# Optimization experiments

Measured on AMD Instinct MI355X. Metric: run time of the kernel, lower is better.

The kernel has to match this reference:

```python
import jax, jax.numpy as jnp
import numpy as np

S = 4096
D_MODEL = 1024
D_INTERNAL = 4096


def setup_inputs() -> dict:
    key = jax.random.key(0)
    ks = jax.random.split(key, 12)
    s = 0.02
    return {
        "x": jax.random.normal(ks[0], (S, D_MODEL), dtype=jnp.float32),
        # projection weights stored as [d_in, d_out] so y = x @ W + b
        "Wq": jax.random.normal(ks[1], (D_MODEL, D_MODEL), dtype=jnp.float32) * s,
        "bq": jnp.zeros((D_MODEL,), dtype=jnp.float32),
        "Wk": jax.random.normal(ks[2], (D_MODEL, D_MODEL), dtype=jnp.float32) * s,
        "bk": jnp.zeros((D_MODEL,), dtype=jnp.float32),
        "Wv": jax.random.normal(ks[3], (D_MODEL, D_MODEL), dtype=jnp.float32) * s,
        "bv": jnp.zeros((D_MODEL,), dtype=jnp.float32),
        "W1": jax.random.normal(ks[4], (D_MODEL, D_INTERNAL), dtype=jnp.float32) * s,
        "b1": jnp.zeros((D_INTERNAL,), dtype=jnp.float32),
        "W2": jax.random.normal(ks[5], (D_INTERNAL, D_MODEL), dtype=jnp.float32) * s,
        "b2": jnp.zeros((D_MODEL,), dtype=jnp.float32),
    }


def reference(x, Wq, bq, Wk, bk, Wv, bv, W1, b1, W2, b2):
    # x: [S, D] (module is unbatched: k.transpose(0,1) implies 2-D input)
    d_model = x.shape[-1]
    q = x @ Wq + bq                         # [S, D]
    k = x @ Wk + bk                         # [S, D]
    v = x @ Wv + bv                         # [S, D]
    scores = (q @ k.T) / jnp.sqrt(jnp.asarray(d_model, x.dtype))  # [S, S]
    s = x.shape[0]
    causal = jnp.triu(jnp.ones((s, s), dtype=bool), k=1)           # True above diag
    scores = jnp.where(causal, jnp.asarray(-1e9, x.dtype), scores)
    attn = jax.nn.softmax(scores, axis=-1)  # [S, S]
    attended = attn @ v                     # [S, D]
    h = x + attended                        # residual 1
    ff = jax.nn.relu(h @ W1 + b1) @ W2 + b2 # 2-layer MLP
    out = h + ff                            # residual 2
    return (out, attn)
```

## Files before the change

### kernel.cpp

```cpp
#include <hip/hip_runtime.h>
#include <hip/hip_bf16.h>


typedef __attribute__((ext_vector_type(4))) float  f32x4;
typedef __attribute__((ext_vector_type(8))) short  bf16x8;
typedef __attribute__((ext_vector_type(4))) unsigned short us4;
typedef __attribute__((ext_vector_type(8))) unsigned short us8;

#define DEVINL __device__ __forceinline__

static constexpr int S   = 4096;
static constexpr int DM  = 1024;
static constexpr int DI  = 4096;

DEVINL unsigned short f2bf(float f) {
  union { float f; unsigned u; } v; v.f = f;
  unsigned r = v.u + 0x7fffu + ((v.u >> 16) & 1u);
  return (unsigned short)(r >> 16);
}

DEVINL float bf2f(unsigned short b) {
  union { unsigned u; float f; } v; v.u = ((unsigned)b) << 16;
  return v.f;
}

DEVINL void gld_lds16(const unsigned short* g, unsigned short* l) {
  __builtin_amdgcn_global_load_lds(
      (const __attribute__((address_space(1))) void*)g,
      (__attribute__((address_space(3))) void*)l,
      16, 0, 0);
}

DEVINL int xcd_remap(int orig, int nwg) {
  const int q = nwg >> 3, r = nwg & 7;
  const int x = orig & 7, idx = orig >> 3;
  return (x < r ? x * (q + 1) : r * (q + 1) + (x - r) * q) + idx;
}

__global__ void prep_all(const float* __restrict__ x,
                         const float* __restrict__ Wq,
                         const float* __restrict__ Wk,
                         const float* __restrict__ Wv,
                         const float* __restrict__ W1,
                         const float* __restrict__ W2,
                         const float* __restrict__ bq,
                         const float* __restrict__ bk,
                         const float* __restrict__ bv,
                         unsigned short* __restrict__ xb,
                         unsigned short* __restrict__ Wqkvt,
                         unsigned short* __restrict__ W1t,
                         unsigned short* __restrict__ W2t,
                         float* __restrict__ bqkv) {
  __shared__ float tile[32][33];
  const int b = blockIdx.x;
  const int tid = threadIdx.x;

  if (b < 2048) {
    long i = ((long)b * 256 + tid) * 8;
    f32x4 a = *(const f32x4*)(x + i);
    f32x4 c = *(const f32x4*)(x + i + 4);
    us8 o;
    o[0] = f2bf(a[0]); o[1] = f2bf(a[1]); o[2] = f2bf(a[2]); o[3] = f2bf(a[3]);
    o[4] = f2bf(c[0]); o[5] = f2bf(c[1]); o[6] = f2bf(c[2]); o[7] = f2bf(c[3]);
    *(us8*)(xb + i) = o;
    return;
  }
  if (b >= 13312) {
    const int t = b - 13312;
    const float* src = (t == 0) ? bq : (t == 1) ? bk : bv;
    const int i = tid * 4;
    *(f32x4*)(bqkv + t * DM + i) = *(const f32x4*)(src + i);
    return;
  }

  const float* in; unsigned short* out; int R, C, t;
  if (b < 3072)      { in = Wq; out = Wqkvt;                      R = DM; C = DM; t = b - 2048; }
  else if (b < 4096) { in = Wk; out = Wqkvt + (size_t)DM * DM;    R = DM; C = DM; t = b - 3072; }
  else if (b < 5120) { in = Wv; out = Wqkvt + 2 * (size_t)DM * DM;R = DM; C = DM; t = b - 4096; }
  else if (b < 9216) { in = W1; out = W1t;                        R = DM; C = DI; t = b - 5120; }
  else               { in = W2; out = W2t;                        R = DI; C = DM; t = b - 9216; }
  const int gx = C >> 5;
  const int bx = (t % gx) * 32, by = (t / gx) * 32;
  const int tx = tid & 31, ty = tid >> 5;
  #pragma unroll
  for (int j = 0; j < 4; ++j) {
    int r = ty + j * 8;
    tile[r][tx] = in[(size_t)(by + r) * C + bx + tx];
  }
  __syncthreads();
  #pragma unroll
  for (int j = 0; j < 4; ++j) {
    int r = ty + j * 8;
    out[(size_t)(bx + r) * R + by + tx] = f2bf(tile[tx][r]);
  }
}

__global__ void transpose_bf16(const unsigned short* __restrict__ in, int ld,
                               unsigned short* __restrict__ out, int ldo) {
  __shared__ unsigned short tile[32][33];
  const int bx = blockIdx.x * 32, by = blockIdx.y * 32;
  const int tx = threadIdx.x, ty = threadIdx.y;
  #pragma unroll
  for (int j = 0; j < 4; ++j) {
    int r = ty + j * 8;
    tile[r][tx] = in[(size_t)(by + r) * ld + bx + tx];
  }
  __syncthreads();
  #pragma unroll
  for (int j = 0; j < 4; ++j) {
    int r = ty + j * 8;
    out[(size_t)(bx + r) * ldo + by + tx] = tile[tx][r];
  }
}

enum { EPI_QKV = 0, EPI_SCE = 1, EPI_FF1 = 4, EPI_PART = 6 };

#define VM_WAIT0 asm volatile("s_waitcnt vmcnt(0)" ::: "memory")

template <int EPI, bool TRI_PACK, bool TRI_TRUNC>
__launch_bounds__(256, 2)
__global__ void gemm4(const unsigned short* __restrict__ A,
                      const unsigned short* __restrict__ Bt,
                      int M, int N, int K, int lda, int ldb, int kChunk, int GX,
                      const float* __restrict__ bias,
                      float* __restrict__ Cf,
                      unsigned short* __restrict__ Cb,
                      float scale) {
  const int wg = xcd_remap(blockIdx.x, gridDim.x);
  int bm, bn;
  if (TRI_PACK) {
    int t = wg;
    bm = (int)((sqrtf(8.f * (float)t + 1.f) - 1.f) * 0.5f);
    while ((bm + 1) * (bm + 2) / 2 <= t) ++bm;
    while (bm * (bm + 1) / 2 > t) --bm;
    bn = t - bm * (bm + 1) / 2;
  } else {
    const int GY_ = gridDim.x / GX;
    const int bpp = GY_ * 8;
    const int panel = wg / bpp, rem = wg % bpp;
    bm = rem >> 3;
    bn = panel * 8 + (rem & 7);
  }
  const int bm0 = bm * 128, bn0 = bn * 128;

  const int kbeg = blockIdx.z * kChunk;
  int kend = min(K, kbeg + kChunk);
  if (TRI_TRUNC) kend = min(kend, bm0 + 128);
  const int len = kend - kbeg;
  const int NT = (len > 0) ? (len >> 6) : 0;

  __shared__ __align__(16) unsigned short lds[2 * 16384];

  const int tid  = threadIdx.x;
  const int lane = tid & 63;
  const int w    = tid >> 6;
  const int wr   = w >> 1, wc = w & 1;
  const int fr   = lane & 15, fq = lane >> 4;

  f32x4 acc[4][4] = {};

  const int tq = tid >> 2;
  const int swcolE = ((tid & 3) * 8) ^ ((tq & 6) << 2);
  const unsigned short* gA = A  + (size_t)(bm0 + tq) * lda + kbeg + swcolE;
  const unsigned short* gB = Bt + (size_t)(bn0 + tq) * ldb + kbeg + swcolE;
  const size_t aH = (size_t)64 * lda, bH = (size_t)64 * ldb;

  auto stage = [&](int buf, int t_) {
    unsigned short* base = (unsigned short*)lds + buf * 16384;
    const size_t go = (size_t)t_ * 64;
    #pragma unroll
    for (int ks = 0; ks < 2; ++ks) {
      const size_t gk = go + ks * 32;
      gld_lds16(gA + gk,      base + ks * 4096 + w * 512);
      gld_lds16(gA + aH + gk, base + ks * 4096 + 2048 + w * 512);
      gld_lds16(gB + gk,      base + 8192 + ks * 4096 + w * 512);
      gld_lds16(gB + bH + gk, base + 8192 + ks * 4096 + 2048 + w * 512);
    }
  };

  const int frSw = (fq * 8) ^ ((fr & 6) << 2);
  auto rdA = [&](int buf, int ks, int mi) {
    return *(const bf16x8*)((const unsigned short*)lds + buf * 16384 + ks * 4096 +
                            (wr * 64 + mi * 16 + fr) * 32 + frSw);
  };
  auto rdB = [&](int buf, int ks, int ni) {
    return *(const bf16x8*)((const unsigned short*)lds + buf * 16384 + 8192 + ks * 4096 +
                            (wc * 64 + ni * 16 + fr) * 32 + frSw);
  };

  if (NT > 0) {
    stage(0, 0);
    VM_WAIT0;
    __builtin_amdgcn_s_barrier();

    for (int t = 0; t < NT; ++t) {
      const int cur = t & 1, nxt = cur ^ 1;
      const bool pf = (t + 1 < NT);
      if (pf) stage(nxt, t + 1);

      #pragma unroll
      for (int ks = 0; ks < 2; ++ks) {
        bf16x8 a[4], b[4];
        #pragma unroll
        for (int mi = 0; mi < 4; ++mi) a[mi] = rdA(cur, ks, mi);
        #pragma unroll
        for (int ni = 0; ni < 4; ++ni) b[ni] = rdB(cur, ks, ni);
        #pragma unroll
        for (int mi = 0; mi < 4; ++mi)
          #pragma unroll
          for (int ni = 0; ni < 4; ++ni)
            acc[mi][ni] = __builtin_amdgcn_mfma_f32_16x16x32_bf16(
                a[mi], b[ni], acc[mi][ni], 0, 0, 0);
      }

      if (pf) { VM_WAIT0; }
      __builtin_amdgcn_s_barrier();
    }
  }

  const int row0 = bm0 + wr * 64 + fq * 4;
  const int col0 = bn0 + wc * 64 + fr;
  const size_t zoff = (EPI == EPI_PART) ? (size_t)blockIdx.z * M * N : 0;
  #pragma unroll
  for (int ni = 0; ni < 4; ++ni) {
    const int col = col0 + ni * 16;
    float bval = 0.f;
    if (EPI == EPI_QKV || EPI == EPI_FF1) bval = bias[col];
    #pragma unroll
    for (int mi = 0; mi < 4; ++mi) {
      #pragma unroll
      for (int j = 0; j < 4; ++j) {
        const int row = row0 + mi * 16 + j;
        const size_t idx = zoff + (size_t)row * N + col;
        const float c = acc[mi][ni][j];
        if (EPI == EPI_QKV) {
          Cb[idx] = f2bf(c + bval);
        } else if (EPI == EPI_SCE) {
          const float e = (col <= row) ? __expf(c * scale) : 0.f;
          Cb[idx] = f2bf(e);
        } else if (EPI == EPI_FF1) {
          const float r = c + bval;
          Cb[idx] = f2bf(r > 0.f ? r : 0.f);
        } else {
          Cf[idx] = c;
        }
      }
    }
  }
}

__global__ void normalize_rows(const unsigned short* __restrict__ attnb,
                               float* __restrict__ attnf,
                               float* __restrict__ rowsum) {
  const int m = blockIdx.x;
  const int tid = threadIdx.x;
  const int valid = m + 1;
  const unsigned short* rowb = attnb + (size_t)m * S;
  float* rowf = attnf + (size_t)m * S;

  float v[4][4];
  float lsum = 0.f;
  #pragma unroll
  for (int i = 0; i < 4; ++i) {
    const int idx = tid * 4 + i * 1024;
    #pragma unroll
    for (int j = 0; j < 4; ++j) v[i][j] = 0.f;
    if (i * 1024 <= m) {
      us4 b = *(const us4*)(rowb + idx);
      #pragma unroll
      for (int j = 0; j < 4; ++j) {
        const float e = (idx + j < valid) ? bf2f(b[j]) : 0.f;
        v[i][j] = e;
        lsum += e;
      }
    }
  }
  #pragma unroll
  for (int off = 32; off > 0; off >>= 1)
    lsum += __shfl_xor(lsum, off, 64);

  __shared__ float red[4];
  if ((tid & 63) == 0) red[tid >> 6] = lsum;
  __syncthreads();
  const float total = red[0] + red[1] + red[2] + red[3];
  if (tid == 0) rowsum[m] = total;
  const float inv = 1.0f / total;

  #pragma unroll
  for (int i = 0; i < 4; ++i) {
    const int idx = tid * 4 + i * 1024;
    f32x4 o;
    #pragma unroll
    for (int j = 0; j < 4; ++j) o[j] = v[i][j] * inv;
    *(f32x4*)(rowf + idx) = o;
  }
}

template <bool FINAL, bool NORM>
__global__ void reduce_k(const float* __restrict__ P,
                         const float* __restrict__ res,
                         const float* __restrict__ bias,
                         const float* __restrict__ rowsum,
                         float* __restrict__ outf,
                         unsigned short* __restrict__ outb, long n) {
  long i = ((long)blockIdx.x * 256 + threadIdx.x) * 4;
  if (i >= n) return;
  f32x4 a = *(const f32x4*)(P + i);
  f32x4 b = *(const f32x4*)(P + n + i);
  f32x4 r = *(const f32x4*)(res + i);
  float inv = 1.f;
  if (NORM) inv = 1.0f / rowsum[i >> 10];
  if (FINAL) {
    f32x4 bb = *(const f32x4*)(bias + (i & (DM - 1)));
    f32x4 o;
    #pragma unroll
    for (int j = 0; j < 4; ++j) o[j] = a[j] + b[j] + r[j] + bb[j];
    *(f32x4*)(outf + i) = o;
  } else {
    f32x4 o; us4 ob;
    #pragma unroll
    for (int j = 0; j < 4; ++j) {
      o[j] = (a[j] + b[j]) * inv + r[j];
      ob[j] = f2bf(o[j]);
    }
    *(f32x4*)(outf + i) = o;
    *(us4*)(outb + i) = ob;
  }
}

extern "C" void kernel_launch(void* const* d_in, const int* in_sizes, int n_in,
                              void* d_out, int out_size, void* d_ws, size_t ws_size,
                              hipStream_t stream) {
  const float* x  = (const float*)d_in[0];
  const float* Wq = (const float*)d_in[1];
  const float* bq = (const float*)d_in[2];
  const float* Wk = (const float*)d_in[3];
  const float* bk = (const float*)d_in[4];
  const float* Wv = (const float*)d_in[5];
  const float* bv = (const float*)d_in[6];
  const float* W1 = (const float*)d_in[7];
  const float* b1 = (const float*)d_in[8];
  const float* W2 = (const float*)d_in[9];
  const float* b2 = (const float*)d_in[10];
  (void)in_sizes; (void)n_in; (void)out_size; (void)ws_size;

  float* outp  = (float*)d_out;
  float* attnf = (float*)d_out + (size_t)S * DM;

  const size_t MB = 1ull << 20;
  char* ws = (char*)d_ws;
  unsigned short* W2t   = (unsigned short*)(ws + 0 * MB);
  unsigned short* W1t   = (unsigned short*)(ws + 8 * MB);
  float*          h     = (float*)(ws + 16 * MB);
  unsigned short* hb    = (unsigned short*)(ws + 32 * MB);
  unsigned short* vt    = (unsigned short*)(ws + 40 * MB);
  unsigned short* attnb = (unsigned short*)(ws + 48 * MB);
  unsigned short* qkv   = (unsigned short*)(ws + 80 * MB);
  unsigned short* xb    = (unsigned short*)(ws + 104 * MB);
  unsigned short* Wqkvt = (unsigned short*)(ws + 112 * MB);
  float*          bqkv  = (float*)(ws + 118 * MB);
  float*          rowsum= (float*)(ws + 119 * MB);
  unsigned short* ff1b  = (unsigned short*)(ws + 40 * MB);
  float*          Ppv   = (float*)(ws + 80 * MB);
  float*          Pff   = (float*)(ws + 72 * MB);

  prep_all<<<dim3(13315), 256, 0, stream>>>(
      x, Wq, Wk, Wv, W1, W2, bq, bk, bv, xb, Wqkvt, W1t, W2t, bqkv);

  gemm4<EPI_QKV, false, false><<<dim3((S / 128) * (3072 / 128), 1, 1), 256, 0, stream>>>(
      xb, Wqkvt, S, 3072, DM, DM, DM, DM, 3072 / 128, bqkv, nullptr, qkv, 1.f);
  transpose_bf16<<<dim3(DM / 32, S / 32), dim3(32, 8), 0, stream>>>(
      qkv + 2 * DM, 3072, vt, S);

  gemm4<EPI_SCE, true, false><<<dim3(528, 1, 1), 256, 0, stream>>>(
      qkv, qkv + DM, S, S, DM, 3072, 3072, DM, 0, nullptr, nullptr, attnb, 0.03125f);

  normalize_rows<<<dim3(S), 256, 0, stream>>>(attnb, attnf, rowsum);

  gemm4<EPI_PART, false, true><<<dim3((S / 128) * (DM / 128), 1, 2), 256, 0, stream>>>(
      attnb, vt, S, DM, S, S, S, S / 2, DM / 128, nullptr, Ppv, nullptr, 1.f);
  reduce_k<false, true><<<dim3((S * DM) / 1024), 256, 0, stream>>>(
      Ppv, x, nullptr, rowsum, h, hb, (long)S * DM);

  gemm4<EPI_FF1, false, false><<<dim3((S / 128) * (DI / 128), 1, 1), 256, 0, stream>>>(
      hb, W1t, S, DI, DM, DM, DM, DM, DI / 128, b1, nullptr, ff1b, 1.f);

  gemm4<EPI_PART, false, false><<<dim3((S / 128) * (DM / 128), 1, 2), 256, 0, stream>>>(
      ff1b, W2t, S, DM, DI, DI, DI, DI / 2, DM / 128, nullptr, Pff, nullptr, 1.f);
  reduce_k<true, false><<<dim3((S * DM) / 1024), 256, 0, stream>>>(
      Pff, h, b2, nullptr, outp, nullptr, (long)S * DM);
}
```

Baseline: 240.9 us.

## Replace 128x128 GEMM with 256x256 8-wave ping-pong pipelined kernel

Grows the GEMM tile from 128x128 with 4 waves to 256x256 with 8 waves. The main loop is split into four sub-phases that interleave LDS reads, staged global-to-LDS loads two tiles ahead, barriers, and MFMA bursts raised with s_setprio. Partial vmcnt waits replace the full drains. The aim is more data reuse per tile and overlap of memory traffic with matrix math. The cost is fewer workgroups (e.g. 136 triangle tiles for scores), more registers and LDS per block, and more barriers per iteration.

```diff
diff --git a/kernel.cpp b/kernel.cpp
--- a/kernel.cpp
+++ b/kernel.cpp
@@ -115,17 +115,20 @@
 
 enum { EPI_QKV = 0, EPI_SCE = 1, EPI_FF1 = 4, EPI_PART = 6 };
 
+#define VM_WAIT6 asm volatile("s_waitcnt vmcnt(6)" ::: "memory")
 #define VM_WAIT0 asm volatile("s_waitcnt vmcnt(0)" ::: "memory")
+#define LGKM0    do { asm volatile("s_waitcnt lgkmcnt(0)" ::: "memory"); \
+                      __builtin_amdgcn_sched_barrier(0); } while (0)
 
 template <int EPI, bool TRI_PACK, bool TRI_TRUNC>
-__launch_bounds__(256, 2)
-__global__ void gemm4(const unsigned short* __restrict__ A,
-                      const unsigned short* __restrict__ Bt,
-                      int M, int N, int K, int lda, int ldb, int kChunk, int GX,
-                      const float* __restrict__ bias,
-                      float* __restrict__ Cf,
-                      unsigned short* __restrict__ Cb,
-                      float scale) {
+__launch_bounds__(512, 2)
+__global__ void gemm8p(const unsigned short* __restrict__ A,
+                       const unsigned short* __restrict__ Bt,
+                       int M, int N, int K, int lda, int ldb, int kChunk, int GX,
+                       const float* __restrict__ bias,
+                       float* __restrict__ Cf,
+                       unsigned short* __restrict__ Cb,
+                       float scale) {
   const int wg = xcd_remap(blockIdx.x, gridDim.x);
   int bm, bn;
   if (TRI_PACK) {
@@ -134,91 +137,125 @@
     while ((bm + 1) * (bm + 2) / 2 <= t) ++bm;
     while (bm * (bm + 1) / 2 > t) --bm;
     bn = t - bm * (bm + 1) / 2;
-  } else {
-    const int GY_ = gridDim.x / GX;
-    const int bpp = GY_ * 8;
-    const int panel = wg / bpp, rem = wg % bpp;
-    bm = rem >> 3;
-    bn = panel * 8 + (rem & 7);
-  }
-  const int bm0 = bm * 128, bn0 = bn * 128;
+  } else { bm = wg / GX; bn = wg % GX; }
+  const int bm0 = bm * 256, bn0 = bn * 256;
 
   const int kbeg = blockIdx.z * kChunk;
   int kend = min(K, kbeg + kChunk);
-  if (TRI_TRUNC) kend = min(kend, bm0 + 128);
-  const int len = kend - kbeg;
-  const int NT = (len > 0) ? (len >> 6) : 0;
-
-  __shared__ __align__(16) unsigned short lds[2 * 16384];
+  if (TRI_TRUNC) kend = min(kend, bm0 + 256);
+  const int NT = (kend > kbeg) ? ((kend - kbeg) >> 6) : 0;
+
+  __shared__ __align__(16) unsigned short lds[2 * 32768];
 
   const int tid  = threadIdx.x;
   const int lane = tid & 63;
   const int w    = tid >> 6;
-  const int wr   = w >> 1, wc = w & 1;
+  const int wr   = w >> 2, wc = w & 3;
   const int fr   = lane & 15, fq = lane >> 4;
 
-  f32x4 acc[4][4] = {};
-
-  const int tq = tid >> 2;
-  const int swcolE = ((tid & 3) * 8) ^ ((tq & 6) << 2);
-  const unsigned short* gA = A  + (size_t)(bm0 + tq) * lda + kbeg + swcolE;
-  const unsigned short* gB = Bt + (size_t)(bn0 + tq) * ldb + kbeg + swcolE;
-  const size_t aH = (size_t)64 * lda, bH = (size_t)64 * ldb;
-
-  auto stage = [&](int buf, int t_) {
-    unsigned short* base = (unsigned short*)lds + buf * 16384;
-    const size_t go = (size_t)t_ * 64;
-    #pragma unroll
-    for (int ks = 0; ks < 2; ++ks) {
-      const size_t gk = go + ks * 32;
-      gld_lds16(gA + gk,      base + ks * 4096 + w * 512);
-      gld_lds16(gA + aH + gk, base + ks * 4096 + 2048 + w * 512);
-      gld_lds16(gB + gk,      base + 8192 + ks * 4096 + w * 512);
-      gld_lds16(gB + bH + gk, base + 8192 + ks * 4096 + 2048 + w * 512);
-    }
+  f32x4 acc[8][4] = {};
+
+  const int srow   = tid >> 2;
+  const int swcolE = ((tid & 3) * 8) ^ ((srow & 6) << 2);
+  const unsigned short* gA = A  + (size_t)(bm0 + srow) * lda + kbeg + swcolE;
+  const unsigned short* gB = Bt + (size_t)(bn0 + srow) * ldb + kbeg + swcolE;
+  const size_t aH = (size_t)128 * lda, bH = (size_t)128 * ldb;
+
+  auto stA = [&](int buf, int t_, int ks) {
+    unsigned short* dst = (unsigned short*)lds + buf * 32768 + ks * 16384 + w * 512;
+    const size_t go = (size_t)t_ * 64 + ks * 32;
+    gld_lds16(gA + go,      dst);
+    gld_lds16(gA + aH + go, dst + 4096);
+  };
+  auto stB = [&](int buf, int t_, int ks) {
+    unsigned short* dst = (unsigned short*)lds + buf * 32768 + 8192 + ks * 16384 + w * 512;
+    const size_t go = (size_t)t_ * 64 + ks * 32;
+    gld_lds16(gB + go,      dst);
+    gld_lds16(gB + bH + go, dst + 4096);
   };
 
   const int frSw = (fq * 8) ^ ((fr & 6) << 2);
   auto rdA = [&](int buf, int ks, int mi) {
-    return *(const bf16x8*)((const unsigned short*)lds + buf * 16384 + ks * 4096 +
-                            (wr * 64 + mi * 16 + fr) * 32 + frSw);
+    return *(const bf16x8*)((const unsigned short*)lds + buf * 32768 + ks * 16384 +
+                            (wr * 128 + mi * 16 + fr) * 32 + frSw);
   };
   auto rdB = [&](int buf, int ks, int ni) {
-    return *(const bf16x8*)((const unsigned short*)lds + buf * 16384 + 8192 + ks * 4096 +
+    return *(const bf16x8*)((const unsigned short*)lds + buf * 32768 + 8192 + ks * 16384 +
                             (wc * 64 + ni * 16 + fr) * 32 + frSw);
   };
 
   if (NT > 0) {
-    stage(0, 0);
-    VM_WAIT0;
+    stA(0, 0, 0); stB(0, 0, 0); stA(0, 0, 1); stB(0, 0, 1);
+    if (NT > 1) { stA(1, 1, 0); stB(1, 1, 0); stA(1, 1, 1); VM_WAIT6; }
+    else        { VM_WAIT0; }
     __builtin_amdgcn_s_barrier();
 
     for (int t = 0; t < NT; ++t) {
-      const int cur = t & 1, nxt = cur ^ 1;
-      const bool pf = (t + 1 < NT);
-      if (pf) stage(nxt, t + 1);
-
-      #pragma unroll
-      for (int ks = 0; ks < 2; ++ks) {
-        bf16x8 a[4], b[4];
-        #pragma unroll
-        for (int mi = 0; mi < 4; ++mi) a[mi] = rdA(cur, ks, mi);
-        #pragma unroll
-        for (int ni = 0; ni < 4; ++ni) b[ni] = rdB(cur, ks, ni);
-        #pragma unroll
-        for (int mi = 0; mi < 4; ++mi)
-          #pragma unroll
-          for (int ni = 0; ni < 4; ++ni)
-            acc[mi][ni] = __builtin_amdgcn_mfma_f32_16x16x32_bf16(
-                a[mi], b[ni], acc[mi][ni], 0, 0, 0);
-      }
-
-      if (pf) { VM_WAIT0; }
+      const int buf = t & 1, nb = buf ^ 1;
+      const bool p1ok = (t + 1 < NT), p2ok = (t + 2 < NT);
+      bf16x8 a[8], b0, b1;
+
+      #pragma unroll
+      for (int mi = 0; mi < 8; ++mi) a[mi] = rdA(buf, 0, mi);
+      b0 = rdB(buf, 0, 0); b1 = rdB(buf, 0, 1);
+      if (p1ok) stB(nb, t + 1, 1);
+      __builtin_amdgcn_s_barrier();
+      LGKM0;
+      __builtin_amdgcn_s_setprio(1);
+      #pragma unroll
+      for (int mi = 0; mi < 8; ++mi) {
+        acc[mi][0] = __builtin_amdgcn_mfma_f32_16x16x32_bf16(a[mi], b0, acc[mi][0], 0, 0, 0);
+        acc[mi][1] = __builtin_amdgcn_mfma_f32_16x16x32_bf16(a[mi], b1, acc[mi][1], 0, 0, 0);
+      }
+      __builtin_amdgcn_s_setprio(0);
+      __builtin_amdgcn_s_barrier();
+
+      b0 = rdB(buf, 0, 2); b1 = rdB(buf, 0, 3);
+      if (p2ok) stA(buf, t + 2, 0);
+      __builtin_amdgcn_s_barrier();
+      LGKM0;
+      __builtin_amdgcn_s_setprio(1);
+      #pragma unroll
+      for (int mi = 0; mi < 8; ++mi) {
+        acc[mi][2] = __builtin_amdgcn_mfma_f32_16x16x32_bf16(a[mi], b0, acc[mi][2], 0, 0, 0);
+        acc[mi][3] = __builtin_amdgcn_mfma_f32_16x16x32_bf16(a[mi], b1, acc[mi][3], 0, 0, 0);
+      }
+      __builtin_amdgcn_s_setprio(0);
+      __builtin_amdgcn_s_barrier();
+
+      #pragma unroll
+      for (int mi = 0; mi < 8; ++mi) a[mi] = rdA(buf, 1, mi);
+      b0 = rdB(buf, 1, 0); b1 = rdB(buf, 1, 1);
+      if (p2ok) stB(buf, t + 2, 0);
+      __builtin_amdgcn_s_barrier();
+      LGKM0;
+      __builtin_amdgcn_s_setprio(1);
+      #pragma unroll
+      for (int mi = 0; mi < 8; ++mi) {
+        acc[mi][0] = __builtin_amdgcn_mfma_f32_16x16x32_bf16(a[mi], b0, acc[mi][0], 0, 0, 0);
+        acc[mi][1] = __builtin_amdgcn_mfma_f32_16x16x32_bf16(a[mi], b1, acc[mi][1], 0, 0, 0);
+      }
+      __builtin_amdgcn_s_setprio(0);
+      __builtin_amdgcn_s_barrier();
+
+      b0 = rdB(buf, 1, 2); b1 = rdB(buf, 1, 3);
+      if (p2ok) stA(buf, t + 2, 1);
+      __builtin_amdgcn_s_barrier();
+      LGKM0;
+      __builtin_amdgcn_s_setprio(1);
+      #pragma unroll
+      for (int mi = 0; mi < 8; ++mi) {
+        acc[mi][2] = __builtin_amdgcn_mfma_f32_16x16x32_bf16(a[mi], b0, acc[mi][2], 0, 0, 0);
+        acc[mi][3] = __builtin_amdgcn_mfma_f32_16x16x32_bf16(a[mi], b1, acc[mi][3], 0, 0, 0);
+      }
+      __builtin_amdgcn_s_setprio(0);
+      if (p2ok)      { VM_WAIT6; }
+      else if (p1ok) { VM_WAIT0; }
       __builtin_amdgcn_s_barrier();
     }
   }
 
-  const int row0 = bm0 + wr * 64 + fq * 4;
+  const int row0 = bm0 + wr * 128 + fq * 4;
   const int col0 = bn0 + wc * 64 + fr;
   const size_t zoff = (EPI == EPI_PART) ? (size_t)blockIdx.z * M * N : 0;
   #pragma unroll
@@ -227,7 +264,7 @@
     float bval = 0.f;
     if (EPI == EPI_QKV || EPI == EPI_FF1) bval = bias[col];
     #pragma unroll
-    for (int mi = 0; mi < 4; ++mi) {
+    for (int mi = 0; mi < 8; ++mi) {
       #pragma unroll
       for (int j = 0; j < 4; ++j) {
         const int row = row0 + mi * 16 + j;
@@ -367,26 +404,26 @@
   prep_all<<<dim3(13315), 256, 0, stream>>>(
       x, Wq, Wk, Wv, W1, W2, bq, bk, bv, xb, Wqkvt, W1t, W2t, bqkv);
 
-  gemm4<EPI_QKV, false, false><<<dim3((S / 128) * (3072 / 128), 1, 1), 256, 0, stream>>>(
-      xb, Wqkvt, S, 3072, DM, DM, DM, DM, 3072 / 128, bqkv, nullptr, qkv, 1.f);
+  gemm8p<EPI_QKV, false, false><<<dim3((S / 256) * (3072 / 256), 1, 1), 512, 0, stream>>>(
+      xb, Wqkvt, S, 3072, DM, DM, DM, DM, 3072 / 256, bqkv, nullptr, qkv, 1.f);
   transpose_bf16<<<dim3(DM / 32, S / 32), dim3(32, 8), 0, stream>>>(
       qkv + 2 * DM, 3072, vt, S);
 
-  gemm4<EPI_SCE, true, false><<<dim3(528, 1, 1), 256, 0, stream>>>(
+  gemm8p<EPI_SCE, true, false><<<dim3(136, 1, 1), 512, 0, stream>>>(
       qkv, qkv + DM, S, S, DM, 3072, 3072, DM, 0, nullptr, nullptr, attnb, 0.03125f);
 
   normalize_rows<<<dim3(S), 256, 0, stream>>>(attnb, attnf, rowsum);
 
-  gemm4<EPI_PART, false, true><<<dim3((S / 128) * (DM / 128), 1, 2), 256, 0, stream>>>(
-      attnb, vt, S, DM, S, S, S, S / 2, DM / 128, nullptr, Ppv, nullptr, 1.f);
+  gemm8p<EPI_PART, false, true><<<dim3((S / 256) * (DM / 256), 1, 2), 512, 0, stream>>>(
+      attnb, vt, S, DM, S, S, S, S / 2, DM / 256, nullptr, Ppv, nullptr, 1.f);
   reduce_k<false, true><<<dim3((S * DM) / 1024), 256, 0, stream>>>(
       Ppv, x, nullptr, rowsum, h, hb, (long)S * DM);
 
-  gemm4<EPI_FF1, false, false><<<dim3((S / 128) * (DI / 128), 1, 1), 256, 0, stream>>>(
-      hb, W1t, S, DI, DM, DM, DM, DM, DI / 128, b1, nullptr, ff1b, 1.f);
-
-  gemm4<EPI_PART, false, false><<<dim3((S / 128) * (DM / 128), 1, 2), 256, 0, stream>>>(
-      ff1b, W2t, S, DM, DI, DI, DI, DI / 2, DM / 128, nullptr, Pff, nullptr, 1.f);
+  gemm8p<EPI_FF1, false, false><<<dim3((S / 256) * (DI / 256), 1, 1), 512, 0, stream>>>(
+      hb, W1t, S, DI, DM, DM, DM, DM, DI / 256, b1, nullptr, ff1b, 1.f);
+
+  gemm8p<EPI_PART, false, false><<<dim3((S / 256) * (DM / 256), 1, 2), 512, 0, stream>>>(
+      ff1b, W2t, S, DM, DI, DI, DI, DI / 2, DM / 256, nullptr, Pff, nullptr, 1.f);
   reduce_k<true, false><<<dim3((S * DM) / 1024), 256, 0, stream>>>(
       Pff, h, b2, nullptr, outp, nullptr, (long)S * DM);
 }
```

Measured after the change: 287.8 us. 19.5% more time.
